# Performance work log

Hardware: AMD Instinct MI355X
Metric: run time of the kernel (lower is better)

## Reference

```python
import jax, jax.numpy as jnp
import numpy as np

# Segment boundaries from the original hard-coded slices: 13,13,13,9,4 repeated twice
SEG_BOUNDS = [0, 13, 26, 39, 48, 52, 65, 78, 91, 100, 104]


def segmented_log_softmax(x):
    # x: [B, 104]; independent log-softmax over each of the 10 fixed segments
    return jnp.concatenate(
        [jax.nn.log_softmax(x[:, a:b], axis=-1)
         for a, b in zip(SEG_BOUNDS[:-1], SEG_BOUNDS[1:])], axis=-1)


def setup_inputs() -> dict:
    key = jax.random.key(0)
    ks = jax.random.split(key, 8)
    B, H, D = 8192, 2048, 104
    return {
        "line": jax.random.normal(ks[0], (B, D), dtype=jnp.float32),
        "hidden": jax.random.normal(ks[1], (B, H), dtype=jnp.float32),
        "U_w": jax.random.normal(ks[2], (H, H), dtype=jnp.float32) * 0.02,
        "U_b": jax.random.normal(ks[3], (H,), dtype=jnp.float32) * 0.02,
        "W_w": jax.random.normal(ks[4], (H, D), dtype=jnp.float32) * 0.02,
        "W_b": jax.random.normal(ks[5], (H,), dtype=jnp.float32) * 0.02,
        "V_w": jax.random.normal(ks[6], (D, H), dtype=jnp.float32) * 0.02,
        "V_b": jax.random.normal(ks[7], (D,), dtype=jnp.float32) * 0.02,
    }


def reference(line, hidden, U_w, U_b, W_w, W_b, V_w, V_b):
    # h_t = sigmoid(U(hidden) + W(line)); torch Linear: y = x @ W.T + b
    h_t = jax.nn.sigmoid(hidden @ U_w.T + U_b + line @ W_w.T + W_b)  # [B, H]
    pred = h_t @ V_w.T + V_b                                          # [B, 104]
    pred_logsoft = segmented_log_softmax(pred)                        # [B, 104]
    return pred_logsoft, h_t
```

## Files before the change

### kernel.cpp

```cpp
#include <hip/hip_runtime.h>
#include <cstdint>
#include <cstddef>


typedef __bf16 bf16x8 __attribute__((ext_vector_type(8)));
typedef float  f32x4  __attribute__((ext_vector_type(4)));
typedef float  f32x16 __attribute__((ext_vector_type(16)));
typedef int    i32x4  __attribute__((ext_vector_type(4)));
typedef int    i32x8  __attribute__((ext_vector_type(8)));
typedef unsigned short ushort8 __attribute__((ext_vector_type(8)));
typedef unsigned char  uchar8  __attribute__((ext_vector_type(8)));
typedef float  float4v __attribute__((ext_vector_type(4)));

#define BB 8192
#define HH 2048
#define DD 104

static __device__ __forceinline__ unsigned short f2bf(float f) {
  unsigned u = __float_as_uint(f);
  unsigned r = (u + 0x7FFFu + ((u >> 16) & 1u)) >> 16;
  return (unsigned short)r;
}

static __device__ __forceinline__ unsigned char f2fp8(float x) {
  unsigned u = __float_as_uint(x);
  unsigned s = (u >> 24) & 0x80u;
  float ax = fabsf(x);
  ax = fminf(ax, 448.0f);
  unsigned code;
  if (ax >= 0.015625f) {
    unsigned b = __float_as_uint(ax);
    unsigned lsb = (b >> 20) & 1u;
    b += 0x0007FFFFu + lsb;
    unsigned e = (b >> 23) & 0xFFu;
    code = ((e - 120u) << 3) | ((b >> 20) & 7u);
  } else {
    code = (unsigned)__float2int_rn(ax * 512.0f);
  }
  return (unsigned char)(s | code);
}

#define GLD_LDS(g, l)                                                          \
  __builtin_amdgcn_global_load_lds(                                            \
      (__attribute__((address_space(1))) void*)(g),                            \
      (__attribute__((address_space(3))) void*)(l), 16, 0, 0)

#define MEMFENCE asm volatile("" ::: "memory")
#define MFMA16(a, b, c) __builtin_amdgcn_mfma_f32_16x16x32_bf16((a), (b), (c), 0, 0, 0)

__global__ __launch_bounds__(256) void prep_kernel(
    const float* __restrict__ hidden, const float* __restrict__ Uw,
    const float* __restrict__ line, const float* __restrict__ Ww,
    const float* __restrict__ Vw,
    unsigned char* __restrict__ out_h, unsigned char* __restrict__ out_u,
    unsigned char* __restrict__ line8, unsigned char* __restrict__ Ww8,
    unsigned short* __restrict__ Vw_bf) {
  const int bid = blockIdx.x;
  if (bid < 10240) {
    long long i = ((long long)bid * blockDim.x + threadIdx.x) * 8;
    const float* src; unsigned char* dst; long long off;
    if (i < (long long)BB * HH) { src = hidden; dst = out_h; off = i; }
    else { src = Uw; dst = out_u; off = i - (long long)BB * HH; }
    float4v a = *(const float4v*)(src + off);
    float4v b = *(const float4v*)(src + off + 4);
    uchar8 o;
    o[0]=f2fp8(a[0]); o[1]=f2fp8(a[1]); o[2]=f2fp8(a[2]); o[3]=f2fp8(a[3]);
    o[4]=f2fp8(b[0]); o[5]=f2fp8(b[1]); o[6]=f2fp8(b[2]); o[7]=f2fp8(b[3]);
    *(uchar8*)(dst + off) = o;
  } else {
    int i = (bid - 10240) * blockDim.x + threadIdx.x;
    const int N1 = BB * 128;
    const int N2 = N1 + HH * 128;
    if (i < N1) {
      int r = i >> 7, c = i & 127;
      line8[i] = (c < DD) ? f2fp8(line[r * DD + c]) : (unsigned char)0;
    } else if (i < N2) {
      int j = i - N1; int r = j >> 7, c = j & 127;
      Ww8[j] = (c < DD) ? f2fp8(Ww[r * DD + c]) : (unsigned char)0;
    } else {
      int j = i - N2; int r = j >> 11, c = j & 2047;
      Vw_bf[j] = (r < DD) ? f2bf(Vw[r * 2048 + c]) : (unsigned short)0;
    }
  }
}

__global__ __launch_bounds__(256, 2) void gemm1_kernel(
    const unsigned char* __restrict__ A8,
    const unsigned char* __restrict__ L8,
    const unsigned char* __restrict__ U8w,
    const unsigned char* __restrict__ W8w,
    const float* __restrict__ Ub, const float* __restrict__ Wb,
    float* __restrict__ outH, unsigned short* __restrict__ outHbf) {
  __shared__ __attribute__((aligned(32))) unsigned char smem[65536];
  const int t = threadIdx.x;
  const int l = t & 63;
  const int wid = t >> 6;
  const int wr = wid >> 1, wc = wid & 1;

  const int bid = blockIdx.x;
  const int wg = (bid & 7) * 128 + (bid >> 3);
  const int brow = (wg >> 4) * 128;
  const int bcol = (wg & 15) * 128;

  const int lr = l & 31;
  const int lc = l >> 5;

  const int sr = t >> 1, sh = (t & 1) * 16;
  const unsigned char* pA = A8 + (size_t)(brow + sr) * 2048 + sh;
  const unsigned char* pL = L8 + (size_t)(brow + sr) * 128 + sh;
  const unsigned char* pU = U8w + (size_t)(bcol + sr) * 2048 + sh;
  const unsigned char* pW = W8w + (size_t)(bcol + sr) * 128 + sh;
  unsigned char* dA = smem + t * 16;
  unsigned char* dB = smem + 32768 + t * 16;

  f32x16 acc[2][2] = {};

  auto stage = [&](int kt, int buf) {
    const int kb = kt * 128;
    unsigned char* da = dA + buf * 16384;
    unsigned char* db = dB + buf * 16384;
    if (kb < 2048) {
#pragma unroll
      for (int q = 0; q < 4; ++q) {
        GLD_LDS(pA + kb + q * 32, da + q * 4096);
        GLD_LDS(pU + kb + q * 32, db + q * 4096);
      }
    } else {
#pragma unroll
      for (int q = 0; q < 4; ++q) {
        GLD_LDS(pL + q * 32, da + q * 4096);
        GLD_LDS(pW + q * 32, db + q * 4096);
      }
    }
  };

  stage(0, 0);
  asm volatile("s_waitcnt vmcnt(0)" ::: "memory");
  MEMFENCE; __builtin_amdgcn_s_barrier(); MEMFENCE;

  for (int kt = 0; kt < 17; ++kt) {
    const int cur = kt & 1;
    if (kt < 16) {
      stage(kt + 1, cur ^ 1);
      asm volatile("s_waitcnt vmcnt(8)" ::: "memory");
    } else {
      asm volatile("s_waitcnt vmcnt(0)" ::: "memory");
    }
    const unsigned char* Ab = smem + cur * 16384;
    const unsigned char* Bb = smem + 32768 + cur * 16384;
#pragma unroll
    for (int s = 0; s < 2; ++s) {
      const int pr = (s * 2 + lc) * 4096;
      i32x8 af[2], bfv[2];
#pragma unroll
      for (int m = 0; m < 2; ++m)
        af[m] = *(const i32x8*)(Ab + pr + (wr * 64 + m * 32 + lr) * 32);
#pragma unroll
      for (int n = 0; n < 2; ++n)
        bfv[n] = *(const i32x8*)(Bb + pr + (wc * 64 + n * 32 + lr) * 32);
      __builtin_amdgcn_s_setprio(1);
#pragma unroll
      for (int m = 0; m < 2; ++m)
#pragma unroll
        for (int n = 0; n < 2; ++n)
          acc[m][n] = __builtin_amdgcn_mfma_scale_f32_32x32x64_f8f6f4(
              af[m], bfv[n], acc[m][n], 0 , 0 ,
              0, 0x7F7F7F7F , 0, 0x7F7F7F7F );
      __builtin_amdgcn_s_setprio(0);
    }
    MEMFENCE; __builtin_amdgcn_s_barrier(); MEMFENCE;
  }

#pragma unroll
  for (int nf = 0; nf < 2; ++nf) {
    const int col = bcol + wc * 64 + nf * 32 + lr;
    const float bias = Ub[col] + Wb[col];
#pragma unroll
    for (int mf = 0; mf < 2; ++mf) {
#pragma unroll
      for (int reg = 0; reg < 16; ++reg) {
        const int row = brow + wr * 64 + mf * 32 + (reg & 3) + 8 * (reg >> 2) + 4 * lc;
        const float v = acc[mf][nf][reg] + bias;
        const float h = 1.0f / (1.0f + __expf(-v));
        const size_t idx = (size_t)row * HH + col;
        outH[idx] = h;
        outHbf[idx] = f2bf(h);
      }
    }
  }
}

template <int NM, int NN>
static __device__ __forceinline__ void mfma_step(
    const unsigned short* sA, const unsigned short* sB, int arow0, int brow0,
    int frow, int fk, f32x4 (&acc)[NM][NN]) {
  bf16x8 af[NM], bfr[NN];
#pragma unroll
  for (int m = 0; m < NM; ++m)
    af[m] = *(const bf16x8*)(sA + (arow0 + m * 16 + frow) * 32 + fk);
#pragma unroll
  for (int n = 0; n < NN; ++n)
    bfr[n] = *(const bf16x8*)(sB + (brow0 + n * 16 + frow) * 32 + fk);
#pragma unroll
  for (int m = 0; m < NM; ++m)
#pragma unroll
    for (int n = 0; n < NN; ++n)
      acc[m][n] = MFMA16(af[m], bfr[n], acc[m][n]);
}

__global__ __launch_bounds__(256, 2) void gemm2_kernel(
    const unsigned short* __restrict__ A,
    const unsigned short* __restrict__ Bm,
    const float* __restrict__ Vb,
    float* __restrict__ outLS) {
  __shared__ unsigned short sA[64 * 32];
  __shared__ unsigned short sB[128 * 32];
  __shared__ float pred[64 * 105];
  const int t = threadIdx.x;
  const int l = t & 63;
  const int wid = t >> 6, wr = wid >> 1, wc = wid & 1;
  const int brow = blockIdx.x * 64;
  const int srow = t >> 2, scg = t & 3;
  const int frow = l & 15, fk = (l >> 4) * 8;

  const unsigned short* gA = A + (size_t)(brow + srow) * HH + scg * 8;
  const unsigned short* gB = Bm + (size_t)srow * HH + scg * 8;
  unsigned short* lA = sA + t * 8;
  unsigned short* lB = sB + t * 8;

  f32x4 acc[2][4] = {};
  for (int ks = 0; ks < 64; ++ks) {
    __syncthreads();
    GLD_LDS(gA, lA);
    GLD_LDS(gB, lB);
    GLD_LDS(gB + 64 * HH, lB + 64 * 32);
    gA += 32; gB += 32;
    __syncthreads();
    mfma_step<2, 4>(sA, sB, wr * 32, wc * 64, frow, fk, acc);
  }

#pragma unroll
  for (int n = 0; n < 4; ++n) {
    const int col = wc * 64 + n * 16 + frow;
    if (col < DD) {
      const float vb = Vb[col];
#pragma unroll
      for (int m = 0; m < 2; ++m) {
        const int r0 = wr * 32 + m * 16 + (l >> 4) * 4;
#pragma unroll
        for (int j = 0; j < 4; ++j)
          pred[(r0 + j) * 105 + col] = acc[m][n][j] + vb;
      }
    }
  }
  __syncthreads();

  if (t < 64) {
    const int segb[11] = {0, 13, 26, 39, 48, 52, 65, 78, 91, 100, 104};
    const float* p = pred + t * 105;
    float* o = outLS + (size_t)(brow + t) * DD;
    for (int s = 0; s < 10; ++s) {
      const int a = segb[s], b = segb[s + 1];
      float mx = -3.0e38f;
      for (int c = a; c < b; ++c) mx = fmaxf(mx, p[c]);
      float sum = 0.0f;
      for (int c = a; c < b; ++c) sum += __expf(p[c] - mx);
      const float ls = __logf(sum) + mx;
      for (int c = a; c < b; ++c) o[c] = p[c] - ls;
    }
  }
}

extern "C" void kernel_launch(void* const* d_in, const int* in_sizes, int n_in,
                              void* d_out, int out_size, void* d_ws, size_t ws_size,
                              hipStream_t stream) {
  (void)in_sizes; (void)n_in; (void)out_size; (void)ws_size;
  const float* line   = (const float*)d_in[0];
  const float* hidden = (const float*)d_in[1];
  const float* Uw     = (const float*)d_in[2];
  const float* Ub     = (const float*)d_in[3];
  const float* Ww     = (const float*)d_in[4];
  const float* Wb     = (const float*)d_in[5];
  const float* Vw     = (const float*)d_in[6];
  const float* Vb     = (const float*)d_in[7];

  char* ws = (char*)d_ws;
  unsigned char* hid8    = (unsigned char*)(ws);
  unsigned char* U8w     = (unsigned char*)(ws + 16777216);
  unsigned char* line8   = (unsigned char*)(ws + 20971520);
  unsigned char* Ww8     = (unsigned char*)(ws + 22020096);
  unsigned short* Vw_bf  = (unsigned short*)(ws + 22282240);
  unsigned short* ht_bf  = (unsigned short*)(ws + 22806528);

  float* outLS = (float*)d_out;
  float* outH  = (float*)d_out + (size_t)BB * DD;

  prep_kernel<<<16384, 256, 0, stream>>>(hidden, Uw, line, Ww, Vw,
                                         hid8, U8w, line8, Ww8, Vw_bf);
  gemm1_kernel<<<1024, 256, 0, stream>>>(hid8, line8, U8w, Ww8, Ub, Wb,
                                         outH, ht_bf);
  gemm2_kernel<<<128, 256, 0, stream>>>(ht_bf, Vw_bf, Vb, outLS);
}
```

Before: 117.1 us.

## Fuse second GEMM into first GEMM epilogue with atomic split-K accumulation

The h_t @ V^T projection now happens inside the gemm1 epilogue. Each 128x128 tile of sigmoid output is written to shared memory as bf16, multiplied against the matching 128-column slice of V, and the partial sums are atomically added into a zeroed fp32 buffer. This removes the bf16 h_t round-trip through global memory and the low-parallelism 128-block gemm2 kernel, which ran a serial 64-step K loop. The cost is many float atomics (16 column tiles per output element), an extra zeroing pass, and a separate small softmax kernel that adds the bias.

```diff
diff --git a/kernel.cpp b/kernel.cpp
--- a/kernel.cpp
+++ b/kernel.cpp
@@ -54,7 +54,7 @@
     const float* __restrict__ Vw,
     unsigned char* __restrict__ out_h, unsigned char* __restrict__ out_u,
     unsigned char* __restrict__ line8, unsigned char* __restrict__ Ww8,
-    unsigned short* __restrict__ Vw_bf) {
+    unsigned short* __restrict__ Vw_bf, float* __restrict__ predP) {
   const int bid = blockIdx.x;
   if (bid < 10240) {
     long long i = ((long long)bid * blockDim.x + threadIdx.x) * 8;
@@ -67,7 +67,7 @@
     o[0]=f2fp8(a[0]); o[1]=f2fp8(a[1]); o[2]=f2fp8(a[2]); o[3]=f2fp8(a[3]);
     o[4]=f2fp8(b[0]); o[5]=f2fp8(b[1]); o[6]=f2fp8(b[2]); o[7]=f2fp8(b[3]);
     *(uchar8*)(dst + off) = o;
-  } else {
+  } else if (bid < 16384) {
     int i = (bid - 10240) * blockDim.x + threadIdx.x;
     const int N1 = BB * 128;
     const int N2 = N1 + HH * 128;
@@ -81,6 +81,10 @@
       int j = i - N2; int r = j >> 11, c = j & 2047;
       Vw_bf[j] = (r < DD) ? f2bf(Vw[r * 2048 + c]) : (unsigned short)0;
     }
+  } else {
+    int i = (bid - 16384) * 256 + threadIdx.x;
+    float4v z = {0.0f, 0.0f, 0.0f, 0.0f};
+    ((float4v*)predP)[i] = z;
   }
 }
 
@@ -89,8 +93,9 @@
     const unsigned char* __restrict__ L8,
     const unsigned char* __restrict__ U8w,
     const unsigned char* __restrict__ W8w,
+    const unsigned short* __restrict__ VwB,
     const float* __restrict__ Ub, const float* __restrict__ Wb,
-    float* __restrict__ outH, unsigned short* __restrict__ outHbf) {
+    float* __restrict__ outH, float* __restrict__ predP) {
   __shared__ __attribute__((aligned(32))) unsigned char smem[65536];
   const int t = threadIdx.x;
   const int l = t & 63;
@@ -171,103 +176,83 @@
     MEMFENCE; __builtin_amdgcn_s_barrier(); MEMFENCE;
   }
 
+  {
+    const unsigned short* pV = VwB + (size_t)(t & 127) * 2048 + bcol + (t >> 7) * 8;
+    unsigned char* dV = smem + 32768 + t * 16;
+#pragma unroll
+    for (int q = 0; q < 8; ++q)
+      GLD_LDS(pV + q * 16, dV + q * 4096);
+  }
 #pragma unroll
   for (int nf = 0; nf < 2; ++nf) {
-    const int col = bcol + wc * 64 + nf * 32 + lr;
+    const int lcol = wc * 64 + nf * 32 + lr;
+    const int col = bcol + lcol;
     const float bias = Ub[col] + Wb[col];
+    unsigned short* hcol = (unsigned short*)smem + (lcol >> 3) * 1024 + (lcol & 7);
 #pragma unroll
     for (int mf = 0; mf < 2; ++mf) {
 #pragma unroll
       for (int reg = 0; reg < 16; ++reg) {
-        const int row = brow + wr * 64 + mf * 32 + (reg & 3) + 8 * (reg >> 2) + 4 * lc;
+        const int lrow = wr * 64 + mf * 32 + (reg & 3) + 8 * (reg >> 2) + 4 * lc;
         const float v = acc[mf][nf][reg] + bias;
         const float h = 1.0f / (1.0f + __expf(-v));
-        const size_t idx = (size_t)row * HH + col;
-        outH[idx] = h;
-        outHbf[idx] = f2bf(h);
-      }
-    }
-  }
-}
-
-template <int NM, int NN>
-static __device__ __forceinline__ void mfma_step(
-    const unsigned short* sA, const unsigned short* sB, int arow0, int brow0,
-    int frow, int fk, f32x4 (&acc)[NM][NN]) {
-  bf16x8 af[NM], bfr[NN];
-#pragma unroll
-  for (int m = 0; m < NM; ++m)
-    af[m] = *(const bf16x8*)(sA + (arow0 + m * 16 + frow) * 32 + fk);
-#pragma unroll
-  for (int n = 0; n < NN; ++n)
-    bfr[n] = *(const bf16x8*)(sB + (brow0 + n * 16 + frow) * 32 + fk);
-#pragma unroll
-  for (int m = 0; m < NM; ++m)
-#pragma unroll
-    for (int n = 0; n < NN; ++n)
-      acc[m][n] = MFMA16(af[m], bfr[n], acc[m][n]);
-}
-
-__global__ __launch_bounds__(256, 2) void gemm2_kernel(
-    const unsigned short* __restrict__ A,
-    const unsigned short* __restrict__ Bm,
-    const float* __restrict__ Vb,
+        outH[(size_t)(brow + lrow) * HH + col] = h;
+        hcol[lrow * 8] = f2bf(h);
+      }
+    }
+  }
+  __syncthreads();
+
+  {
+    const int frow = l & 15, fk = l >> 4;
+    f32x4 acc2[4][4] = {};
+#pragma unroll
+    for (int ks = 0; ks < 4; ++ks) {
+      const int g = ks * 4 + fk;
+      bf16x8 av[4], bv[4];
+#pragma unroll
+      for (int mi = 0; mi < 4; ++mi)
+        av[mi] = *(const bf16x8*)(smem + g * 2048 + (wr * 64 + mi * 16 + frow) * 16);
+#pragma unroll
+      for (int ni = 0; ni < 4; ++ni)
+        bv[ni] = *(const bf16x8*)(smem + 32768 + g * 2048 + (wc * 64 + ni * 16 + frow) * 16);
+#pragma unroll
+      for (int mi = 0; mi < 4; ++mi)
+#pragma unroll
+        for (int ni = 0; ni < 4; ++ni)
+          acc2[mi][ni] = MFMA16(av[mi], bv[ni], acc2[mi][ni]);
+    }
+#pragma unroll
+    for (int ni = 0; ni < 4; ++ni) {
+      const int d = wc * 64 + ni * 16 + frow;
+      if (d < DD) {
+#pragma unroll
+        for (int mi = 0; mi < 4; ++mi) {
+          const int r0 = brow + wr * 64 + mi * 16 + fk * 4;
+#pragma unroll
+          for (int j = 0; j < 4; ++j)
+            atomicAdd(&predP[(size_t)(r0 + j) * DD + d], acc2[mi][ni][j]);
+        }
+      }
+    }
+  }
+}
+
+__global__ __launch_bounds__(256) void softmax_kernel(
+    const float* __restrict__ predP, const float* __restrict__ Vb,
     float* __restrict__ outLS) {
-  __shared__ unsigned short sA[64 * 32];
-  __shared__ unsigned short sB[128 * 32];
-  __shared__ float pred[64 * 105];
-  const int t = threadIdx.x;
-  const int l = t & 63;
-  const int wid = t >> 6, wr = wid >> 1, wc = wid & 1;
-  const int brow = blockIdx.x * 64;
-  const int srow = t >> 2, scg = t & 3;
-  const int frow = l & 15, fk = (l >> 4) * 8;
-
-  const unsigned short* gA = A + (size_t)(brow + srow) * HH + scg * 8;
-  const unsigned short* gB = Bm + (size_t)srow * HH + scg * 8;
-  unsigned short* lA = sA + t * 8;
-  unsigned short* lB = sB + t * 8;
-
-  f32x4 acc[2][4] = {};
-  for (int ks = 0; ks < 64; ++ks) {
-    __syncthreads();
-    GLD_LDS(gA, lA);
-    GLD_LDS(gB, lB);
-    GLD_LDS(gB + 64 * HH, lB + 64 * 32);
-    gA += 32; gB += 32;
-    __syncthreads();
-    mfma_step<2, 4>(sA, sB, wr * 32, wc * 64, frow, fk, acc);
-  }
-
-#pragma unroll
-  for (int n = 0; n < 4; ++n) {
-    const int col = wc * 64 + n * 16 + frow;
-    if (col < DD) {
-      const float vb = Vb[col];
-#pragma unroll
-      for (int m = 0; m < 2; ++m) {
-        const int r0 = wr * 32 + m * 16 + (l >> 4) * 4;
-#pragma unroll
-        for (int j = 0; j < 4; ++j)
-          pred[(r0 + j) * 105 + col] = acc[m][n][j] + vb;
-      }
-    }
-  }
-  __syncthreads();
-
-  if (t < 64) {
-    const int segb[11] = {0, 13, 26, 39, 48, 52, 65, 78, 91, 100, 104};
-    const float* p = pred + t * 105;
-    float* o = outLS + (size_t)(brow + t) * DD;
-    for (int s = 0; s < 10; ++s) {
-      const int a = segb[s], b = segb[s + 1];
-      float mx = -3.0e38f;
-      for (int c = a; c < b; ++c) mx = fmaxf(mx, p[c]);
-      float sum = 0.0f;
-      for (int c = a; c < b; ++c) sum += __expf(p[c] - mx);
-      const float ls = __logf(sum) + mx;
-      for (int c = a; c < b; ++c) o[c] = p[c] - ls;
-    }
+  const int r = blockIdx.x * 256 + threadIdx.x;
+  const float* p = predP + (size_t)r * DD;
+  float* o = outLS + (size_t)r * DD;
+  const int segb[11] = {0, 13, 26, 39, 48, 52, 65, 78, 91, 100, 104};
+  for (int s = 0; s < 10; ++s) {
+    const int a = segb[s], b = segb[s + 1];
+    float mx = -3.0e38f;
+    for (int c = a; c < b; ++c) mx = fmaxf(mx, p[c] + Vb[c]);
+    float sum = 0.0f;
+    for (int c = a; c < b; ++c) sum += __expf(p[c] + Vb[c] - mx);
+    const float ls = __logf(sum) + mx;
+    for (int c = a; c < b; ++c) o[c] = p[c] + Vb[c] - ls;
   }
 }
 
@@ -290,14 +275,14 @@
   unsigned char* line8   = (unsigned char*)(ws + 20971520);
   unsigned char* Ww8     = (unsigned char*)(ws + 22020096);
   unsigned short* Vw_bf  = (unsigned short*)(ws + 22282240);
-  unsigned short* ht_bf  = (unsigned short*)(ws + 22806528);
+  float* predP           = (float*)(ws + 22806528);
 
   float* outLS = (float*)d_out;
   float* outH  = (float*)d_out + (size_t)BB * DD;
 
-  prep_kernel<<<16384, 256, 0, stream>>>(hidden, Uw, line, Ww, Vw,
-                                         hid8, U8w, line8, Ww8, Vw_bf);
-  gemm1_kernel<<<1024, 256, 0, stream>>>(hid8, line8, U8w, Ww8, Ub, Wb,
-                                         outH, ht_bf);
-  gemm2_kernel<<<128, 256, 0, stream>>>(ht_bf, Vw_bf, Vb, outLS);
-}
+  prep_kernel<<<17216, 256, 0, stream>>>(hidden, Uw, line, Ww, Vw,
+                                         hid8, U8w, line8, Ww8, Vw_bf, predP);
+  gemm1_kernel<<<1024, 256, 0, stream>>>(hid8, line8, U8w, Ww8, Vw_bf, Ub, Wb,
+                                         outH, predP);
+  softmax_kernel<<<32, 256, 0, stream>>>(predP, Vb, outLS);
+}
```

Result: slower. 158.6 us (+35.5%).
